# Kernel optimization log

Measured on AMD Instinct MI355X. Metric: run time of the kernel, lower is better.

Reference implementation:

```python
import jax, jax.numpy as jnp
import numpy as np

NUM_HEADS = 16
WINDOW = 128


def apply_rope(x):
    # x: (B, H, S, Dh), standard RoPE with half-split rotation, base 10000
    S, Dh = x.shape[-2], x.shape[-1]
    half = Dh // 2
    inv_freq = 1.0 / (10000.0 ** (jnp.arange(half, dtype=jnp.float32) / half))
    ang = jnp.arange(S, dtype=jnp.float32)[:, None] * inv_freq[None, :]  # (S, half)
    cos, sin = jnp.cos(ang), jnp.sin(ang)
    x1, x2 = x[..., :half], x[..., half:]
    return jnp.concatenate([x1 * cos - x2 * sin, x1 * sin + x2 * cos], axis=-1).astype(x.dtype)


def setup_inputs() -> dict:
    key = jax.random.key(0)
    ks = jax.random.split(key, 5)
    D = 1024
    B, S = 2, 2048
    w = 0.02
    return {
        "x": jax.random.normal(ks[0], (B, S, D), dtype=jnp.float32),
        "Wq": jax.random.normal(ks[1], (D, D), dtype=jnp.float32) * w,
        "bq": jnp.zeros((D,), dtype=jnp.float32),
        "Wk": jax.random.normal(ks[2], (D, D), dtype=jnp.float32) * w,
        "bk": jnp.zeros((D,), dtype=jnp.float32),
        "Wv": jax.random.normal(ks[3], (D, D), dtype=jnp.float32) * w,
        "bv": jnp.zeros((D,), dtype=jnp.float32),
        "Wo": jax.random.normal(ks[4], (D, D), dtype=jnp.float32) * w,
        "bo": jnp.zeros((D,), dtype=jnp.float32),
    }


def reference(x, Wq, bq, Wk, bk, Wv, bv, Wo, bo):
    B, S, D = x.shape
    H = NUM_HEADS
    Dh = D // H

    def proj(W, b):
        y = jnp.einsum("bsd,ed->bse", x, W) + b  # nn.Linear: x @ W.T + b
        return y.reshape(B, S, H, Dh).transpose(0, 2, 1, 3)  # (B,H,S,Dh)

    q = apply_rope(proj(Wq, bq)) * (Dh ** -0.5)
    k = apply_rope(proj(Wk, bk))
    v = proj(Wv, bv)

    scores = jnp.einsum("bhqd,bhkd->bhqk", q, k)  # (B,H,S,S)
    idx = jnp.arange(S)
    rel = idx[None, :] - idx[:, None]  # k - q
    blocked = (rel > 0) | (rel < -WINDOW)  # True = masked out
    scores = jnp.where(blocked[None, None], -jnp.inf, scores)
    probs = jax.nn.softmax(scores, axis=-1)
    out = jnp.einsum("bhqk,bhkd->bhqd", probs, v)
    out = out.transpose(0, 2, 1, 3).reshape(B, S, D)
    return jnp.einsum("bsd,ed->bse", out, Wo) + bo
```

## Files before the change

kernel.cpp:

```cpp
#include <hip/hip_runtime.h>

typedef __attribute__((ext_vector_type(8)))  __bf16 bf16x8;
typedef __attribute__((ext_vector_type(4)))  float  f32x4;

__device__ __forceinline__ short f2bf(float f) {
    unsigned u = __builtin_bit_cast(unsigned, f);
    unsigned r = (u + 0x7fffu + ((u >> 16) & 1u)) >> 16;
    return (short)r;
}
__device__ __forceinline__ float lo16(unsigned u) { return __builtin_bit_cast(float, u << 16); }
__device__ __forceinline__ float hi16(unsigned u) { return __builtin_bit_cast(float, u & 0xffff0000u); }

__device__ __forceinline__ void gload16(const void* g, void* l) {
    __builtin_amdgcn_global_load_lds(
        (const __attribute__((address_space(1))) unsigned*)g,
        (__attribute__((address_space(3))) unsigned*)l, 16, 0, 0);
}

__device__ __forceinline__ void ropePair(const uint4& a, const uint4& b,
                                         const float2* cs8, float scale,
                                         uint4& oa, uint4& ob) {
    const unsigned au[4] = {a.x, a.y, a.z, a.w}, bu[4] = {b.x, b.y, b.z, b.w};
    unsigned ra[4], rb[4];
    #pragma unroll
    for (int wi = 0; wi < 4; ++wi) {
        const float x1l = lo16(au[wi]), x1h = hi16(au[wi]);
        const float x2l = lo16(bu[wi]), x2h = hi16(bu[wi]);
        const float2 cl = cs8[wi * 2], ch = cs8[wi * 2 + 1];
        const float o1l = (x1l * cl.x - x2l * cl.y) * scale;
        const float o2l = (x1l * cl.y + x2l * cl.x) * scale;
        const float o1h = (x1h * ch.x - x2h * ch.y) * scale;
        const float o2h = (x1h * ch.y + x2h * ch.x) * scale;
        ra[wi] = (unsigned)(unsigned short)f2bf(o1l) | ((unsigned)(unsigned short)f2bf(o1h) << 16);
        rb[wi] = (unsigned)(unsigned short)f2bf(o2l) | ((unsigned)(unsigned short)f2bf(o2h) << 16);
    }
    oa = make_uint4(ra[0], ra[1], ra[2], ra[3]);
    ob = make_uint4(rb[0], rb[1], rb[2], rb[3]);
}

#define S_LEN   2048
#define MAT_ELEMS 4194304
#define VT_ROW  2176
#define VT_MAT  2228224

__global__ __launch_bounds__(256) void prep(
    const float* __restrict__ x,  const float* __restrict__ Wq,
    const float* __restrict__ Wk, const float* __restrict__ Wv,
    const float* __restrict__ Wo, const float* __restrict__ bq,
    const float* __restrict__ bk, const float* __restrict__ bv,
    short* __restrict__ xb, short* __restrict__ wcat, short* __restrict__ wob,
    float* __restrict__ bcat, float2* __restrict__ tab, short* __restrict__ vt)
{
    const int tid = blockIdx.x * 256 + threadIdx.x;
    const float4* src;
    short* dst;
    if (tid < 1048576) {
        src = (const float4*)x + tid;  dst = xb + (size_t)tid * 4;
    } else if (tid < 1835008) {
        const int o = tid - 1048576;
        const int mat = o >> 18;
        const int wi  = o & 262143;
        const float* W = (mat == 0) ? Wq : (mat == 1) ? Wk : Wv;
        src = (const float4*)W + wi;  dst = wcat + (size_t)o * 4;
    } else {
        const int o = tid - 1835008;
        src = (const float4*)Wo + o;  dst = wob + (size_t)o * 4;
    }
    const float4 v = *src;
    short4 s4 = make_short4(f2bf(v.x), f2bf(v.y), f2bf(v.z), f2bf(v.w));
    *(short4*)dst = s4;

    if (tid < 65536) {
        const int s  = tid >> 5;
        const int jr = tid & 31;
        const float freq = exp2f(-(float)jr * (13.287712379549449f / 32.0f));
        const float ang  = (float)s * freq;
        tab[tid] = make_float2(cosf(ang), sinf(ang));
    }
    if (tid < 768) {
        const float* B = (tid < 256) ? bq : (tid < 512) ? bk : bv;
        ((float4*)bcat)[tid] = ((const float4*)B)[tid & 255];
    }
    if (tid < 16384) {
        const int row = tid >> 3, ch = tid & 7;
        *(uint4*)&vt[(size_t)row * VT_ROW + ch * 8] = make_uint4(0, 0, 0, 0);
    }
}

#define VMC4 do { asm volatile("s_waitcnt vmcnt(4)" ::: "memory"); __builtin_amdgcn_sched_barrier(0); } while (0)
#define VMC0 do { asm volatile("s_waitcnt vmcnt(0)" ::: "memory"); __builtin_amdgcn_sched_barrier(0); } while (0)
#define BAR  __builtin_amdgcn_s_barrier()

#define LOADA(T, PM)                                                      \
  _Pragma("unroll") for (int ii = 0; ii < 4; ++ii) {                      \
    af[ii][0] = ldf(T, fA0, (ii * 32 + (PM) * 128) * 128);                \
    af[ii][1] = ldf(T, fA1, (ii * 32 + (PM) * 128) * 128);                \
  }

#define LOADB(T, PN, BQ)                                                  \
  _Pragma("unroll") for (int jj = 0; jj < 2; ++jj) {                      \
    BQ[jj][0] = ldf(T, fB0, (jj * 64 + (PN) * 128) * 128);                \
    BQ[jj][1] = ldf(T, fB1, (jj * 64 + (PN) * 128) * 128);                \
  }

#define MFMAQ(PM, PN, BQ)                                                     \
  __builtin_amdgcn_s_setprio(1);                                              \
  _Pragma("unroll") for (int ii = 0; ii < 4; ++ii)                            \
    _Pragma("unroll") for (int jj = 0; jj < 2; ++jj) {                        \
      acc[(PM)*4+ii][(PN)*2+jj] = __builtin_amdgcn_mfma_f32_16x16x32_bf16(    \
          af[ii][0], BQ[jj][0], acc[(PM)*4+ii][(PN)*2+jj], 0, 0, 0);          \
      acc[(PM)*4+ii][(PN)*2+jj] = __builtin_amdgcn_mfma_f32_16x16x32_bf16(    \
          af[ii][1], BQ[jj][1], acc[(PM)*4+ii][(PN)*2+jj], 0, 0, 0);          \
    }                                                                         \
  __builtin_amdgcn_s_setprio(0);

#define KTILE(AC, BC, S1, S2, S3, S4, W4)                                 \
  LOADA(AC, 0); LOADB(BC, 0, bq0); S1; BAR; MFMAQ(0, 0, bq0); BAR;        \
  LOADB(BC, 1, bq1); S2; BAR; MFMAQ(0, 1, bq1); BAR;                      \
  LOADA(AC, 1); S3; BAR; MFMAQ(1, 0, bq0); BAR;                           \
  S4; BAR; MFMAQ(1, 1, bq1); W4; BAR;

#define STG(G, KT_, H, TILE)                                               \
  { gload16(G + (H) * 262144 + 0     + (KT_) * 128, TILE + ((H)*128 + w*16    ) * 64); \
    gload16(G + (H) * 262144 + 16384 + (KT_) * 128, TILE + ((H)*128 + w*16 + 8) * 64); }

__global__ __launch_bounds__(512) void gemm8(
    const short* __restrict__ A,
    const short* __restrict__ Bw,
    const float* __restrict__ bias,
    short* __restrict__ outb,
    short* __restrict__ vt)
{
    __shared__ short lds[65536];
    short* const Ab0 = lds;
    short* const Bb0 = lds + 16384;
    short* const Ab1 = lds + 32768;
    short* const Bb1 = lds + 49152;

    const int tid = threadIdx.x;
    const int w = tid >> 6, lane = tid & 63;
    const int wm = w >> 2, wn = w & 3;
    const int lr = lane & 15, lg = lane >> 4;

    const int wg  = blockIdx.x;
    const int swz = (wg & 7) * 24 + (wg >> 3);
    const int bx = swz % 12, by = swz / 12;
    const int row0 = by * 256, col0 = bx * 256;

    const int scl  = ((lane & 7) * 16) ^ (((lane >> 3) & 7) << 4);
    const int goff = (w * 16 + (lane >> 3)) * 2048 + scl;
    const char* gA = (const char*)A  + (size_t)row0 * 2048 + goff;
    const char* gB = (const char*)Bw + (size_t)col0 * 2048 + goff;
    const int cswz0 = (lg * 16)      ^ ((lr & 7) << 4);
    const int cswz1 = (64 + lg * 16) ^ ((lr & 7) << 4);
    const int fA0 = (wm * 16 + lr) * 128 + cswz0;
    const int fA1 = (wm * 16 + lr) * 128 + cswz1;
    const int fB0 = (wn * 16 + lr) * 128 + cswz0;
    const int fB1 = (wn * 16 + lr) * 128 + cswz1;

    auto ldf = [&](const short* buf, int voff, int imm) -> bf16x8 {
        return *(const bf16x8*)((const char*)buf + voff + imm);
    };

    f32x4 acc[8][4] = {};
    bf16x8 af[4][2], bq0[2][2], bq1[2][2];

    STG(gA, 0, 0, Ab0);  STG(gB, 0, 0, Bb0);
    STG(gA, 0, 1, Ab0);  STG(gB, 0, 1, Bb0);
    STG(gA, 1, 0, Ab1);  STG(gB, 1, 0, Bb1);
    VMC4;
    BAR;

    #pragma unroll 1
    for (int it = 0; it < 7; ++it) {
        const int t0 = it * 2;
        KTILE(Ab0, Bb0,
              STG(gA, t0 + 1, 1, Ab1),
              STG(gB, t0 + 1, 1, Bb1),
              STG(gA, t0 + 2, 0, Ab0),
              STG(gB, t0 + 2, 0, Bb0), VMC4);
        const int t1 = t0 + 1;
        KTILE(Ab1, Bb1,
              STG(gA, t1 + 1, 1, Ab0),
              STG(gB, t1 + 1, 1, Bb0),
              STG(gA, t1 + 2, 0, Ab1),
              STG(gB, t1 + 2, 0, Bb1), VMC4);
    }
    KTILE(Ab0, Bb0,
          STG(gA, 15, 1, Ab1),
          STG(gB, 15, 1, Bb1), {}, {}, VMC0);
    KTILE(Ab1, Bb1, {}, {}, {}, {}, {});

    const int mat = col0 >> 10;
    const int cm0 = col0 & 1023;
    if (mat == 2) {
        #pragma unroll
        for (int j = 0; j < 4; ++j) {
            const int co = wn * 16 + (j & 1) * 64 + (j >> 1) * 128 + lr;
            const float bb = bias[col0 + co];
            const size_t dgo = (size_t)(cm0 + co) * VT_ROW;
            #pragma unroll
            for (int i = 0; i < 8; ++i) {
                const int rg = row0 + wm * 16 + (i & 3) * 32 + (i >> 2) * 128 + lg * 4;
                const int bq_ = rg >> 11, key = rg & 2047;
                short4 sv;
                sv.x = f2bf(acc[i][j][0] + bb); sv.y = f2bf(acc[i][j][1] + bb);
                sv.z = f2bf(acc[i][j][2] + bb); sv.w = f2bf(acc[i][j][3] + bb);
                *(short4*)&vt[(size_t)bq_ * VT_MAT + dgo + 128 + key] = sv;
            }
        }
    } else {
        short* outm = outb + (size_t)mat * MAT_ELEMS;
        #pragma unroll
        for (int j = 0; j < 4; ++j) {
            const int co = wn * 16 + (j & 1) * 64 + (j >> 1) * 128 + lr;
            const float bb = bias[col0 + co];
            #pragma unroll
            for (int i = 0; i < 8; ++i) {
                const int rg = row0 + wm * 16 + (i & 3) * 32 + (i >> 2) * 128 + lg * 4;
                #pragma unroll
                for (int r = 0; r < 4; ++r)
                    outm[(size_t)(rg + r) * 1024 + cm0 + co] = f2bf(acc[i][j][r] + bb);
            }
        }
    }
}

__global__ __launch_bounds__(256) void gemm_out(
    const short* __restrict__ A, const short* __restrict__ Bw,
    const float* __restrict__ bias, float* __restrict__ outf)
{
    __shared__ short As[128 * 64];
    __shared__ short Bs[64 * 64];
    const int tid  = threadIdx.x;
    const int w    = tid >> 6, lane = tid & 63;
    const int row0 = blockIdx.y * 128, col0 = blockIdx.x * 64;
    const int lr   = lane & 15, lg = lane >> 4;
    const int srow = lane >> 3, scol = (lane & 7) * 8;

    f32x4 acc[2][4] = {};

    for (int kt = 0; kt < 16; ++kt) {
        const int k0 = kt * 64;
        __syncthreads();
        #pragma unroll
        for (int rr = 0; rr < 4; ++rr) {
            const int r = w * 32 + rr * 8;
            gload16(A + (size_t)(row0 + r + srow) * 1024 + k0 + scol, (short*)As + r * 64);
        }
        #pragma unroll
        for (int rr = 0; rr < 2; ++rr) {
            const int r = w * 16 + rr * 8;
            gload16(Bw + (size_t)(col0 + r + srow) * 1024 + k0 + scol, (short*)Bs + r * 64);
        }
        __syncthreads();
        #pragma unroll
        for (int kk = 0; kk < 2; ++kk) {
            const int kb = kk * 32 + lg * 8;
            bf16x8 af[2], bf[4];
            #pragma unroll
            for (int i = 0; i < 2; ++i)
                af[i] = *(const bf16x8*)&As[(w * 32 + i * 16 + lr) * 64 + kb];
            #pragma unroll
            for (int j = 0; j < 4; ++j)
                bf[j] = *(const bf16x8*)&Bs[(j * 16 + lr) * 64 + kb];
            #pragma unroll
            for (int i = 0; i < 2; ++i)
                #pragma unroll
                for (int j = 0; j < 4; ++j)
                    acc[i][j] = __builtin_amdgcn_mfma_f32_16x16x32_bf16(af[i], bf[j], acc[i][j], 0, 0, 0);
        }
    }

    #pragma unroll
    for (int i = 0; i < 2; ++i) {
        const int grb = row0 + w * 32 + i * 16 + lg * 4;
        #pragma unroll
        for (int j = 0; j < 4; ++j) {
            const int cm = col0 + j * 16 + lr;
            const float bb = bias[cm];
            #pragma unroll
            for (int r = 0; r < 4; ++r)
                outf[(size_t)(grb + r) * 1024 + cm] = acc[i][j][r] + bb;
        }
    }
}

#define KS_ST 72
#define P_ST  168
__global__ __launch_bounds__(256) void attn_mfma(const short* __restrict__ qkv,
                                                 const short* __restrict__ vt,
                                                 short* __restrict__ ctx,
                                                 const float2* __restrict__ tab)
{
    __shared__ char lds[52736];
    short* Ks  = (short*)lds;
    short* Pl  = (short*)lds;
    char*  VTs = lds + 27648;
    float* linv = (float*)(lds + 52480);

    const int tid = threadIdx.x;
    const int w = tid >> 6, lane = tid & 63;
    const int g = lane >> 4, l15 = lane & 15;
    const int phys = blockIdx.x;
    const int bid = (phys & 7) * 128 + (phys >> 3);
    const int b  = bid >> 9;
    const int h  = (bid >> 5) & 15;
    const int qb = bid & 31;
    const int qs = qb << 6;
    const size_t rowbase = (size_t)b * S_LEN;
    const int hc = h << 6;

    const short* vhead = vt + ((size_t)b * 1024 + h * 64) * VT_ROW + qs;
    #pragma unroll
    for (int rdx = 0; rdx < 6; ++rdx) {
        const int c = rdx * 256 + tid;
        const int row = c / 24, ch = c - row * 24;
        const int srcb = (ch * 16) ^ ((row & 7) << 4);
        gload16((const char*)(vhead + (size_t)row * VT_ROW) + srcb, VTs + c * 16);
    }

    #pragma unroll
    for (int it = 0; it < 3; ++it) {
        const int c   = it * 256 + tid;
        const int key = c >> 2;
        const int jb  = (c & 3) << 3;
        const int gk  = qs - 128 + key;
        const int gkc = gk < 0 ? 0 : gk;
        const short* kb = qkv + (size_t)1 * MAT_ELEMS + (rowbase + gkc) * 1024 + hc;
        const uint4 k1 = *(const uint4*)(kb + jb);
        const uint4 k2 = *(const uint4*)(kb + jb + 32);
        uint4 o1, o2;
        ropePair(k1, k2, tab + (size_t)gkc * 32 + jb, 1.0f, o1, o2);
        if (gk < 0) { o1 = make_uint4(0, 0, 0, 0); o2 = make_uint4(0, 0, 0, 0); }
        *(uint4*)&Ks[key * KS_ST + jb]      = o1;
        *(uint4*)&Ks[key * KS_ST + jb + 32] = o2;
    }
    __syncthreads();

    const int q = qs + 16 * w + l15;
    const size_t qoff = (rowbase + q) * 1024 + hc;
    const uint4 q1 = *(const uint4*)&qkv[qoff + g * 8];
    const uint4 q2 = *(const uint4*)&qkv[qoff + 32 + g * 8];
    uint4 r1, r2;
    ropePair(q1, q2, tab + (size_t)q * 32 + g * 8, 0.125f, r1, r2);
    const bf16x8 qf0 = __builtin_bit_cast(bf16x8, r1);
    const bf16x8 qf1 = __builtin_bit_cast(bf16x8, r2);

    f32x4 st[9];
    #pragma unroll
    for (int t = 0; t < 9; ++t) {
        const int krow = 16 * w + 16 * t + l15;
        bf16x8 kf0 = *(const bf16x8*)&Ks[krow * KS_ST + g * 8];
        bf16x8 kf1 = *(const bf16x8*)&Ks[krow * KS_ST + 32 + g * 8];
        f32x4 a = {0.f, 0.f, 0.f, 0.f};
        a = __builtin_amdgcn_mfma_f32_16x16x32_bf16(qf0, kf0, a, 0, 0, 0);
        a = __builtin_amdgcn_mfma_f32_16x16x32_bf16(qf1, kf1, a, 0, 0, 0);
        st[t] = a;
    }
    __syncthreads();

    const int jmin = 128 - qs - 16 * w;
    float mrow[4], lsum[4];
    #pragma unroll
    for (int r = 0; r < 4; ++r) mrow[r] = -3.0e38f;
    #pragma unroll
    for (int t = 0; t < 9; ++t) {
        const int jj = 16 * t + l15;
        #pragma unroll
        for (int r = 0; r < 4; ++r) {
            const int qi = 4 * g + r;
            const bool ok = (jj >= qi) && (jj <= qi + 128) && (jj >= jmin);
            if (ok) mrow[r] = fmaxf(mrow[r], st[t][r]);
        }
    }
    #pragma unroll
    for (int r = 0; r < 4; ++r) {
        mrow[r] = fmaxf(mrow[r], __shfl_xor(mrow[r], 1));
        mrow[r] = fmaxf(mrow[r], __shfl_xor(mrow[r], 2));
        mrow[r] = fmaxf(mrow[r], __shfl_xor(mrow[r], 4));
        mrow[r] = fmaxf(mrow[r], __shfl_xor(mrow[r], 8));
        lsum[r] = 0.0f;
    }
    short* Pw = Pl + w * (16 * P_ST);
    #pragma unroll
    for (int t = 0; t < 9; ++t) {
        const int jj = 16 * t + l15;
        #pragma unroll
        for (int r = 0; r < 4; ++r) {
            const int qi = 4 * g + r;
            const bool ok = (jj >= qi) && (jj <= qi + 128) && (jj >= jmin);
            const float p = ok ? __expf(st[t][r] - mrow[r]) : 0.0f;
            lsum[r] += p;
            Pw[qi * P_ST + jj] = f2bf(p);
        }
    }
    {
        short4 z = make_short4(0, 0, 0, 0);
        *(short4*)&Pw[l15 * P_ST + 144 + 4 * g] = z;
    }
    #pragma unroll
    for (int r = 0; r < 4; ++r) {
        lsum[r] += __shfl_xor(lsum[r], 1);
        lsum[r] += __shfl_xor(lsum[r], 2);
        lsum[r] += __shfl_xor(lsum[r], 4);
        lsum[r] += __shfl_xor(lsum[r], 8);
        if (l15 == r) linv[w * 16 + 4 * g + r] = 1.0f / lsum[r];
    }

    f32x4 oc[4] = {};
    #pragma unroll
    for (int kc = 0; kc < 5; ++kc) {
        bf16x8 pf = *(const bf16x8*)&Pw[l15 * P_ST + kc * 32 + g * 8];
        const int colb = (16 * w + kc * 32 + g * 8) * 2;
        #pragma unroll
        for (int dt = 0; dt < 4; ++dt) {
            const int row = dt * 16 + l15;
            bf16x8 vf = *(const bf16x8*)(VTs + row * 384 + (colb ^ ((row & 7) << 4)));
            oc[dt] = __builtin_amdgcn_mfma_f32_16x16x32_bf16(vf, pf, oc[dt], 0, 0, 0);
        }
    }

    const float inv = linv[w * 16 + l15];
    #pragma unroll
    for (int dt = 0; dt < 4; ++dt) {
        short4 sv;
        sv.x = f2bf(oc[dt][0] * inv);
        sv.y = f2bf(oc[dt][1] * inv);
        sv.z = f2bf(oc[dt][2] * inv);
        sv.w = f2bf(oc[dt][3] * inv);
        *(short4*)&ctx[(rowbase + qs + 16 * w + l15) * 1024 + hc + dt * 16 + 4 * g] = sv;
    }
}

extern "C" void kernel_launch(void* const* d_in, const int* in_sizes, int n_in,
                              void* d_out, int out_size, void* d_ws, size_t ws_size,
                              hipStream_t stream) {
    const float* x  = (const float*)d_in[0];
    const float* Wq = (const float*)d_in[1];
    const float* bq = (const float*)d_in[2];
    const float* Wk = (const float*)d_in[3];
    const float* bk = (const float*)d_in[4];
    const float* Wv = (const float*)d_in[5];
    const float* bv = (const float*)d_in[6];
    const float* Wo = (const float*)d_in[7];
    const float* bo = (const float*)d_in[8];

    char* ws = (char*)d_ws;
    short*  xb   = (short*) (ws + 0);
    short*  ctx  = (short*) (ws + 0);
    short*  wcat = (short*) (ws + 8388608);
    short*  wob  = (short*) (ws + 14680064);
    short*  qkv  = (short*) (ws + 16777216);
    short*  vt   = (short*) (ws + 33554432);
    float2* tab  = (float2*)(ws + 42467328);
    float*  bcat = (float*) (ws + 42991616);

    prep<<<8192, 256, 0, stream>>>(x, Wq, Wk, Wv, Wo, bq, bk, bv,
                                   xb, wcat, wob, bcat, tab, vt);
    gemm8<<<192, 512, 0, stream>>>(xb, wcat, bcat, qkv, vt);
    attn_mfma<<<1024, 256, 0, stream>>>(qkv, vt, ctx, tab);
    gemm_out<<<dim3(16, 32), 256, 0, stream>>>(ctx, wob, bo, (float*)d_out);
}
```

Measured before the change: 88.19 us.

## Retile QKV GEMM to 256x192 tiles so 256 blocks fill all CUs

```diff
diff --git a/kernel.cpp b/kernel.cpp
--- a/kernel.cpp
+++ b/kernel.cpp
@@ -90,39 +90,40 @@
 #define VMC4 do { asm volatile("s_waitcnt vmcnt(4)" ::: "memory"); __builtin_amdgcn_sched_barrier(0); } while (0)
 #define VMC0 do { asm volatile("s_waitcnt vmcnt(0)" ::: "memory"); __builtin_amdgcn_sched_barrier(0); } while (0)
 #define BAR  __builtin_amdgcn_s_barrier()
-
-#define LOADA(T, PM)                                                      \
-  _Pragma("unroll") for (int ii = 0; ii < 4; ++ii) {                      \
-    af[ii][0] = ldf(T, fA0, (ii * 32 + (PM) * 128) * 128);                \
-    af[ii][1] = ldf(T, fA1, (ii * 32 + (PM) * 128) * 128);                \
-  }
-
-#define LOADB(T, PN, BQ)                                                  \
-  _Pragma("unroll") for (int jj = 0; jj < 2; ++jj) {                      \
-    BQ[jj][0] = ldf(T, fB0, (jj * 64 + (PN) * 128) * 128);                \
-    BQ[jj][1] = ldf(T, fB1, (jj * 64 + (PN) * 128) * 128);                \
-  }
-
-#define MFMAQ(PM, PN, BQ)                                                     \
+#define SB   __builtin_amdgcn_sched_barrier(0)
+
+#define LDA_ALL(T) _Pragma("unroll") for (int ii = 0; ii < 4; ++ii) { \
+    aF[ii][0] = ldf(T, fA0, ii * 2048);                                \
+    aF[ii][1] = ldf(T, fA1, ii * 2048); }
+#define LDB0(T) _Pragma("unroll") for (int jj = 0; jj < 3; ++jj) {    \
+    b0[jj][0] = ldf(T, fB0, jj * 2048);                                \
+    b0[jj][1] = ldf(T, fB1, jj * 2048); }
+#define LDB1(T) _Pragma("unroll") for (int jj = 0; jj < 3; ++jj) {    \
+    b1[jj][0] = ldf(T, fB0, (jj + 3) * 2048);                          \
+    b1[jj][1] = ldf(T, fB1, (jj + 3) * 2048); }
+
+#define MFMA_HALF(JB, BQ)                                                     \
   __builtin_amdgcn_s_setprio(1);                                              \
   _Pragma("unroll") for (int ii = 0; ii < 4; ++ii)                            \
-    _Pragma("unroll") for (int jj = 0; jj < 2; ++jj) {                        \
-      acc[(PM)*4+ii][(PN)*2+jj] = __builtin_amdgcn_mfma_f32_16x16x32_bf16(    \
-          af[ii][0], BQ[jj][0], acc[(PM)*4+ii][(PN)*2+jj], 0, 0, 0);          \
-      acc[(PM)*4+ii][(PN)*2+jj] = __builtin_amdgcn_mfma_f32_16x16x32_bf16(    \
-          af[ii][1], BQ[jj][1], acc[(PM)*4+ii][(PN)*2+jj], 0, 0, 0);          \
+    _Pragma("unroll") for (int jj = 0; jj < 3; ++jj) {                        \
+      acc[ii][(JB)+jj] = __builtin_amdgcn_mfma_f32_16x16x32_bf16(             \
+          aF[ii][0], BQ[jj][0], acc[ii][(JB)+jj], 0, 0, 0);                   \
+      acc[ii][(JB)+jj] = __builtin_amdgcn_mfma_f32_16x16x32_bf16(             \
+          aF[ii][1], BQ[jj][1], acc[ii][(JB)+jj], 0, 0, 0);                   \
     }                                                                         \
   __builtin_amdgcn_s_setprio(0);
 
-#define KTILE(AC, BC, S1, S2, S3, S4, W4)                                 \
-  LOADA(AC, 0); LOADB(BC, 0, bq0); S1; BAR; MFMAQ(0, 0, bq0); BAR;        \
-  LOADB(BC, 1, bq1); S2; BAR; MFMAQ(0, 1, bq1); BAR;                      \
-  LOADA(AC, 1); S3; BAR; MFMAQ(1, 0, bq0); BAR;                           \
-  S4; BAR; MFMAQ(1, 1, bq1); W4; BAR;
-
-#define STG(G, KT_, H, TILE)                                               \
-  { gload16(G + (H) * 262144 + 0     + (KT_) * 128, TILE + ((H)*128 + w*16    ) * 64); \
-    gload16(G + (H) * 262144 + 16384 + (KT_) * 128, TILE + ((H)*128 + w*16 + 8) * 64); }
+#define STGA(KT_, TILE) _Pragma("unroll") for (int g = 0; g < 4; ++g)  \
+    gload16(gA + g * 16384 + (KT_) * 128, (TILE) + (w * 32 + g * 8) * 64);
+#define STGB(KT_, TILE) _Pragma("unroll") for (int g = 0; g < 3; ++g)  \
+    gload16(gB + g * 16384 + (KT_) * 128, (TILE) + (w * 24 + g * 8) * 64);
+
+#define KT2(CA, CB, SBSTG, SASTG, WSTMT)              \
+  LDA_ALL(CA); LDB0(CB); SBSTG;                       \
+  MFMA_HALF(0, b0); SB; LDB1(CB); SB;                 \
+  BAR;                                                \
+  SASTG;                                              \
+  MFMA_HALF(3, b1); WSTMT; BAR;
 
 __global__ __launch_bounds__(512) void gemm8(
     const short* __restrict__ A,
@@ -131,96 +132,79 @@
     short* __restrict__ outb,
     short* __restrict__ vt)
 {
-    __shared__ short lds[65536];
+    __shared__ short lds[57344];
     short* const Ab0 = lds;
     short* const Bb0 = lds + 16384;
-    short* const Ab1 = lds + 32768;
-    short* const Bb1 = lds + 49152;
+    short* const Ab1 = lds + 28672;
+    short* const Bb1 = lds + 45056;
 
     const int tid = threadIdx.x;
     const int w = tid >> 6, lane = tid & 63;
-    const int wm = w >> 2, wn = w & 3;
+    const int wm = w >> 1, wn = w & 1;
     const int lr = lane & 15, lg = lane >> 4;
 
     const int wg  = blockIdx.x;
-    const int swz = (wg & 7) * 24 + (wg >> 3);
-    const int bx = swz % 12, by = swz / 12;
-    const int row0 = by * 256, col0 = bx * 256;
+    const int swz = (wg & 7) * 32 + (wg >> 3);
+    const int bx = swz & 15, by = swz >> 4;
+    const int row0 = by * 256, col0 = bx * 192;
 
     const int scl  = ((lane & 7) * 16) ^ (((lane >> 3) & 7) << 4);
-    const int goff = (w * 16 + (lane >> 3)) * 2048 + scl;
-    const char* gA = (const char*)A  + (size_t)row0 * 2048 + goff;
-    const char* gB = (const char*)Bw + (size_t)col0 * 2048 + goff;
+    const int goff = (lane >> 3) * 2048 + scl;
+    const char* gA = (const char*)A  + (size_t)(row0 + w * 32) * 2048 + goff;
+    const char* gB = (const char*)Bw + (size_t)(col0 + w * 24) * 2048 + goff;
     const int cswz0 = (lg * 16)      ^ ((lr & 7) << 4);
     const int cswz1 = (64 + lg * 16) ^ ((lr & 7) << 4);
-    const int fA0 = (wm * 16 + lr) * 128 + cswz0;
-    const int fA1 = (wm * 16 + lr) * 128 + cswz1;
-    const int fB0 = (wn * 16 + lr) * 128 + cswz0;
-    const int fB1 = (wn * 16 + lr) * 128 + cswz1;
+    const int fA0 = (wm * 64 + lr) * 128 + cswz0;
+    const int fA1 = (wm * 64 + lr) * 128 + cswz1;
+    const int fB0 = (wn * 96 + lr) * 128 + cswz0;
+    const int fB1 = (wn * 96 + lr) * 128 + cswz1;
 
     auto ldf = [&](const short* buf, int voff, int imm) -> bf16x8 {
         return *(const bf16x8*)((const char*)buf + voff + imm);
     };
 
-    f32x4 acc[8][4] = {};
-    bf16x8 af[4][2], bq0[2][2], bq1[2][2];
-
-    STG(gA, 0, 0, Ab0);  STG(gB, 0, 0, Bb0);
-    STG(gA, 0, 1, Ab0);  STG(gB, 0, 1, Bb0);
-    STG(gA, 1, 0, Ab1);  STG(gB, 1, 0, Bb1);
+    f32x4 acc[4][6] = {};
+    bf16x8 aF[4][2], b0[3][2], b1[3][2];
+
+    STGA(0, Ab0); STGB(0, Bb0); STGA(1, Ab1);
     VMC4;
     BAR;
 
     #pragma unroll 1
     for (int it = 0; it < 7; ++it) {
         const int t0 = it * 2;
-        KTILE(Ab0, Bb0,
-              STG(gA, t0 + 1, 1, Ab1),
-              STG(gB, t0 + 1, 1, Bb1),
-              STG(gA, t0 + 2, 0, Ab0),
-              STG(gB, t0 + 2, 0, Bb0), VMC4);
+        KT2(Ab0, Bb0, STGB(t0 + 1, Bb1), STGA(t0 + 2, Ab0), VMC4)
         const int t1 = t0 + 1;
-        KTILE(Ab1, Bb1,
-              STG(gA, t1 + 1, 1, Ab0),
-              STG(gB, t1 + 1, 1, Bb0),
-              STG(gA, t1 + 2, 0, Ab1),
-              STG(gB, t1 + 2, 0, Bb1), VMC4);
-    }
-    KTILE(Ab0, Bb0,
-          STG(gA, 15, 1, Ab1),
-          STG(gB, 15, 1, Bb1), {}, {}, VMC0);
-    KTILE(Ab1, Bb1, {}, {}, {}, {}, {});
-
-    const int mat = col0 >> 10;
-    const int cm0 = col0 & 1023;
-    if (mat == 2) {
-        #pragma unroll
-        for (int j = 0; j < 4; ++j) {
-            const int co = wn * 16 + (j & 1) * 64 + (j >> 1) * 128 + lr;
-            const float bb = bias[col0 + co];
-            const size_t dgo = (size_t)(cm0 + co) * VT_ROW;
-            #pragma unroll
-            for (int i = 0; i < 8; ++i) {
-                const int rg = row0 + wm * 16 + (i & 3) * 32 + (i >> 2) * 128 + lg * 4;
+        KT2(Ab1, Bb1, STGB(t1 + 1, Bb0), STGA(t1 + 2, Ab1), VMC4)
+    }
+    KT2(Ab0, Bb0, STGB(15, Bb1), {}, VMC0)
+    KT2(Ab1, Bb1, {}, {}, {})
+
+    #pragma unroll
+    for (int j = 0; j < 6; ++j) {
+        const int base_cm = col0 + wn * 96 + j * 16;
+        const int matj = base_cm >> 10;
+        const float bb = bias[base_cm + lr];
+        if (matj == 2) {
+            const size_t dgo = (size_t)(base_cm - 2048 + lr) * VT_ROW;
+            #pragma unroll
+            for (int i = 0; i < 4; ++i) {
+                const int rg = row0 + wm * 64 + i * 16 + lg * 4;
                 const int bq_ = rg >> 11, key = rg & 2047;
                 short4 sv;
                 sv.x = f2bf(acc[i][j][0] + bb); sv.y = f2bf(acc[i][j][1] + bb);
                 sv.z = f2bf(acc[i][j][2] + bb); sv.w = f2bf(acc[i][j][3] + bb);
                 *(short4*)&vt[(size_t)bq_ * VT_MAT + dgo + 128 + key] = sv;
             }
-        }
-    } else {
-        short* outm = outb + (size_t)mat * MAT_ELEMS;
-        #pragma unroll
-        for (int j = 0; j < 4; ++j) {
-            const int co = wn * 16 + (j & 1) * 64 + (j >> 1) * 128 + lr;
-            const float bb = bias[col0 + co];
-            #pragma unroll
-            for (int i = 0; i < 8; ++i) {
-                const int rg = row0 + wm * 16 + (i & 3) * 32 + (i >> 2) * 128 + lg * 4;
+        } else {
+            short* outm = outb + (size_t)matj * MAT_ELEMS;
+            const int cmod = (base_cm & 1023) + lr;
+            #pragma unroll
+            for (int i = 0; i < 4; ++i) {
+                const int rg = row0 + wm * 64 + i * 16 + lg * 4;
                 #pragma unroll
                 for (int r = 0; r < 4; ++r)
-                    outm[(size_t)(rg + r) * 1024 + cm0 + co] = f2bf(acc[i][j][r] + bb);
+                    outm[(size_t)(rg + r) * 1024 + cmod] = f2bf(acc[i][j][r] + bb);
             }
         }
     }
@@ -458,7 +442,7 @@
 
     prep<<<8192, 256, 0, stream>>>(x, Wq, Wk, Wv, Wo, bq, bk, bv,
                                    xb, wcat, wob, bcat, tab, vt);
-    gemm8<<<192, 512, 0, stream>>>(xb, wcat, bcat, qkv, vt);
+    gemm8<<<256, 512, 0, stream>>>(xb, wcat, bcat, qkv, vt);
     attn_mfma<<<1024, 256, 0, stream>>>(qkv, vt, ctx, tab);
     gemm_out<<<dim3(16, 32), 256, 0, stream>>>(ctx, wob, bo, (float*)d_out);
 }
```

New measurement: 84.15 us. 4.6% less time.
